# Kernel tuning notes

Hardware: AMD Instinct MI355X
Metric: run time of the kernel (lower is better)

Reference implementation:

```python
import jax, jax.numpy as jnp
import numpy as np

H = 97
IN = 9
N_NODES = 100000
N_EDGES = 800000
N_GRAPHS = 4096
N_LAYERS = 7
N_STEPS = 7
BN_EPS = 1e-5


def setup_inputs() -> dict:
    key = jax.random.key(0)
    ks = iter(jax.random.split(key, 40))
    sc = 0.1  # param init scale
    inp = {}
    inp['x'] = jax.random.normal(next(ks), (N_NODES, IN), jnp.float32)
    inp['edge_index'] = jax.random.randint(next(ks), (2, N_EDGES), 0, N_NODES, jnp.int32)
    inp['batch'] = jnp.sort(jax.random.randint(next(ks), (N_NODES,), 0, N_GRAPHS, jnp.int32))
    inp['num_graphs'] = N_GRAPHS
    inp['lin1_W'] = jax.random.normal(next(ks), (IN, H), jnp.float32) * sc
    inp['lin1_b'] = jax.random.normal(next(ks), (H,), jnp.float32) * sc
    for nm in ['Wk', 'Wq', 'Wv', 'Ws']:
        inp['conv_' + nm] = jax.random.normal(next(ks), (N_LAYERS, H, H), jnp.float32) * sc
    for nm in ['bk', 'bq', 'bv', 'bs']:
        inp['conv_' + nm] = jax.random.normal(next(ks), (N_LAYERS, H), jnp.float32) * sc
    inp['gru_Wih'] = jax.random.normal(next(ks), (N_LAYERS, H, 3 * H), jnp.float32) * sc
    inp['gru_Whh'] = jax.random.normal(next(ks), (N_LAYERS, H, 3 * H), jnp.float32) * sc
    inp['gru_bih'] = jax.random.normal(next(ks), (N_LAYERS, 3 * H), jnp.float32) * sc
    inp['gru_bhh'] = jax.random.normal(next(ks), (N_LAYERS, 3 * H), jnp.float32) * sc
    inp['bn_gamma'] = jnp.ones((N_LAYERS - 1, H), jnp.float32)
    inp['bn_beta'] = jnp.zeros((N_LAYERS - 1, H), jnp.float32)
    inp['bn_mean'] = jnp.zeros((N_LAYERS - 1, H), jnp.float32)
    inp['bn_var'] = jnp.ones((N_LAYERS - 1, H), jnp.float32)
    inp['gat_W'] = jax.random.normal(next(ks), (H, H), jnp.float32) * sc
    inp['gat_asrc'] = jax.random.normal(next(ks), (H,), jnp.float32) * sc
    inp['gat_adst'] = jax.random.normal(next(ks), (H,), jnp.float32) * sc
    inp['gat_b'] = jax.random.normal(next(ks), (H,), jnp.float32) * sc
    inp['molgru_Wih'] = jax.random.normal(next(ks), (H, 3 * H), jnp.float32) * sc
    inp['molgru_Whh'] = jax.random.normal(next(ks), (H, 3 * H), jnp.float32) * sc
    inp['molgru_bih'] = jax.random.normal(next(ks), (3 * H,), jnp.float32) * sc
    inp['molgru_bhh'] = jax.random.normal(next(ks), (3 * H,), jnp.float32) * sc
    inp['lin2_W'] = jax.random.normal(next(ks), (H, 1), jnp.float32) * sc
    inp['lin2_b'] = jax.random.normal(next(ks), (1,), jnp.float32) * sc
    return inp


def _gru(xin, h, Wih, Whh, bih, bhh):
    gi = xin @ Wih + bih  # [N, 3H]
    gh = h @ Whh + bhh
    ir, iz, inn = jnp.split(gi, 3, axis=-1)
    hr, hz, hn = jnp.split(gh, 3, axis=-1)
    r = jax.nn.sigmoid(ir + hr)
    z = jax.nn.sigmoid(iz + hz)
    n = jnp.tanh(inn + r * hn)
    return (1.0 - z) * n + z * h


def _resgated(x, src, dst, Wk, bk, Wq, bq, Wv, bv, Ws, bs, n_nodes):
    # PyG ResGatedGraphConv: out_i = Ws x_i + sum_j sigmoid(Wk x_i + Wq x_j) * (Wv x_j)
    k = x @ Wk + bk
    q = x @ Wq + bq
    v = x @ Wv + bv
    msg = jax.nn.sigmoid(k[dst] + q[src]) * v[src]  # [E, H]
    agg = jax.ops.segment_sum(msg, dst, num_segments=n_nodes)
    return agg + (x @ Ws + bs)


def _forward(x, lin1_W, lin1_b, conv_Wk, conv_bk, conv_Wq, conv_bq, conv_Wv, conv_bv,
             conv_Ws, conv_bs, gru_Wih, gru_Whh, gru_bih, gru_bhh,
             bn_gamma, bn_beta, bn_mean, bn_var,
             gat_W, gat_asrc, gat_adst, gat_b,
             molgru_Wih, molgru_Whh, molgru_bih, molgru_bhh,
             lin2_W, lin2_b, edge_index, batch, num_graphs):
    src, dst = edge_index[0], edge_index[1]
    n_nodes = x.shape[0]
    x = jax.nn.leaky_relu(x @ lin1_W + lin1_b, 0.01)
    # layer 0 (gate_conv + gru)
    h = jax.nn.elu(_resgated(x, src, dst, conv_Wk[0], conv_bk[0], conv_Wq[0], conv_bq[0],
                             conv_Wv[0], conv_bv[0], conv_Ws[0], conv_bs[0], n_nodes))
    x = jax.nn.relu(_gru(h, x, gru_Wih[0], gru_Whh[0], gru_bih[0], gru_bhh[0]))
    # layers 1..6 with eval-mode BatchNorm (dropout inactive in eval)
    for l in range(1, N_LAYERS):
        h = jax.nn.elu(_resgated(x, src, dst, conv_Wk[l], conv_bk[l], conv_Wq[l], conv_bq[l],
                                 conv_Wv[l], conv_bv[l], conv_Ws[l], conv_bs[l], n_nodes))
        b = l - 1
        h = (h - bn_mean[b]) * (bn_gamma[b] / jnp.sqrt(bn_var[b] + BN_EPS)) + bn_beta[b]
        x = jax.nn.relu(_gru(h, x, gru_Wih[l], gru_Whh[l], gru_bih[l], gru_bhh[l]))
    # molecule readout: global_add_pool then bipartite GAT (heads=1) over node->graph edges
    out = jax.nn.relu(jax.ops.segment_sum(x, batch, num_segments=num_graphs))  # [G, H]
    xs = x @ gat_W          # source projections, fixed over timesteps
    a_s = xs @ gat_asrc     # [N]
    for _ in range(N_STEPS):
        a_d = (out @ gat_W) @ gat_adst  # [G]
        alpha = jax.nn.leaky_relu(a_s + a_d[batch], 0.01)  # one score per node-edge
        m = jax.ops.segment_max(alpha, batch, num_segments=num_graphs)
        m = jnp.where(jnp.isfinite(m), m, 0.0)
        e = jnp.exp(alpha - m[batch])
        s = jax.ops.segment_sum(e, batch, num_segments=num_graphs)
        w = e / s[batch]  # segment softmax over each graph's nodes
        hg = jax.ops.segment_sum(w[:, None] * xs, batch, num_segments=num_graphs) + gat_b
        h = jax.nn.elu(hg)
        out = jax.nn.relu(_gru(h, out, molgru_Wih, molgru_Whh, molgru_bih, molgru_bhh))
    return out @ lin2_W + lin2_b  # [G, 1]


def reference(x, edge_index, batch, num_graphs, lin1_W, lin1_b, conv_Wk, conv_bk, conv_Wq,
              conv_bq, conv_Wv, conv_bv, conv_Ws, conv_bs, gru_Wih, gru_Whh, gru_bih, gru_bhh,
              bn_gamma, bn_beta, bn_mean, bn_var, gat_W, gat_asrc, gat_adst, gat_b,
              molgru_Wih, molgru_Whh, molgru_bih, molgru_bhh, lin2_W, lin2_b):
    return _forward(x, lin1_W, lin1_b, conv_Wk, conv_bk, conv_Wq, conv_bq, conv_Wv, conv_bv,
                    conv_Ws, conv_bs, gru_Wih, gru_Whh, gru_bih, gru_bhh,
                    bn_gamma, bn_beta, bn_mean, bn_var,
                    gat_W, gat_asrc, gat_adst, gat_b,
                    molgru_Wih, molgru_Whh, molgru_bih, molgru_bhh,
                    lin2_W, lin2_b, edge_index, batch, num_graphs)
```

## Files before the change

### kernel.cpp

```cpp
#include <hip/hip_runtime.h>

#define NN 100000
#define NNP 100032
#define NE 800000
#define NG 4096
#define HH 97
#define HP 128
#define NB 391

#define WGF_SET_STRIDE 147456
#define WCF_LAYER_STRIDE 98304

typedef unsigned short u16;
typedef unsigned int u32;
typedef __attribute__((ext_vector_type(8))) short short8v;
typedef __attribute__((ext_vector_type(4))) float f32x4;

__device__ __forceinline__ float sigm_(float x){ return 1.f/(1.f+__expf(-x)); }
__device__ __forceinline__ float lrelu01_(float x){ return x>0.f? x : 0.01f*x; }
__device__ __forceinline__ float tanh_(float t){ float e2=__expf(2.f*t); return 1.f-2.f/(e2+1.f); }
__device__ __forceinline__ float b2f(u16 u){ union{u32 i; float f;} t; t.i=(u32)u<<16; return t.f; }
__device__ __forceinline__ u16 f2b(float x){ union{float f; u32 i;} t; t.f=x; u32 r=t.i+0x7FFFu+((t.i>>16)&1u); return (u16)(r>>16); }

__device__ __forceinline__ f32x4 mfma16(short8v a, short8v b, f32x4 c){
  return __builtin_amdgcn_mfma_f32_16x16x32_bf16(a, b, c, 0, 0, 0);
}

__global__ void k_pack_convw(const float* __restrict__ Wk, const float* __restrict__ Wq,
                             const float* __restrict__ Wv, const float* __restrict__ Ws,
                             u16* __restrict__ out){
  int idx = blockIdx.x*256 + threadIdx.x;
  if (idx >= 7*4*8*3*2*512) return;
  int e = idx & 7, lane = (idx>>3) & 63;
  int r = idx >> 9;
  int term = r & 1; r >>= 1;
  int ks = r % 3; r /= 3;
  int t = r & 7; r >>= 3;
  int w = r & 3; int l = r >> 2;
  int k = ks*32 + (lane>>4)*8 + e;
  int n = (w*8 + t)*16 + (lane & 15);
  int m = n>>7, h = n & 127;
  float val = 0.f;
  if (k < HH && h < HH){
    const float* W = (m==0)? Wk : (m==1)? Wq : (m==2)? Wv : Ws;
    val = W[l*9409 + k*97 + h];
  }
  u16 hi = f2b(val);
  out[idx] = (term==0)? hi : f2b(val - b2f(hi));
}

__global__ void k_pack_gruw(const float* __restrict__ gih, const float* __restrict__ ghh,
                            const float* __restrict__ mih, const float* __restrict__ mhh,
                            u16* __restrict__ out){
  int idx = blockIdx.x*256 + threadIdx.x;
  if (idx >= 8*8*3*3*4*512) return;
  int e = idx & 7, lane = (idx>>3) & 63;
  int r = idx >> 9;
  int mat = r & 3; r >>= 2;
  int ks = r % 3; r /= 3;
  int j = r % 3; r /= 3;
  int bt = r & 7; int set = r >> 3;
  int k = ks*32 + (lane>>4)*8 + e;
  int n = (j*8 + bt)*16 + (lane & 15);
  int jg = n>>7, g = n & 127;
  float val = 0.f;
  if (k < HH && g < HH){
    const float* srcp;
    if (mat < 2) srcp = (set < 7)? gih + (size_t)set*28227 : mih;
    else         srcp = (set < 7)? ghh + (size_t)set*28227 : mhh;
    val = srcp[k*291 + jg*97 + g];
  }
  u16 hi = f2b(val);
  out[idx] = ((mat & 1)==0)? hi : f2b(val - b2f(hi));
}

__global__ void k_pack_gatw(const float* __restrict__ gatW, u16* __restrict__ out){
  int idx = blockIdx.x*256 + threadIdx.x;
  if (idx >= 2*4*8*512) return;
  int e = idx & 7, lane = (idx>>3) & 63, t = (idx>>9) & 7;
  int ks = (idx>>12) & 3, term = idx>>14;
  int k = ks*32 + (lane>>4)*8 + e;
  int h = t*16 + (lane & 15);
  float val = (k < HH && h < HH)? gatW[k*97 + h] : 0.f;
  u16 hi = f2b(val);
  out[idx] = (term==0)? hi : f2b(val - b2f(hi));
}

__global__ void k_pack_w96(const float* __restrict__ Wk, const float* __restrict__ Wq,
                           const float* __restrict__ Wv, const float* __restrict__ Ws,
                           const float* __restrict__ gih, const float* __restrict__ ghh,
                           const float* __restrict__ mih, const float* __restrict__ mhh,
                           float* __restrict__ out){
  int idx = blockIdx.x*256 + threadIdx.x;
  if (idx < 7*512){
    int l = idx >> 9, c = idx & 511;
    int m = c >> 7, h = c & 127;
    float v = 0.f;
    if (h < HH){
      const float* W = (m==0)? Wk : (m==1)? Wq : (m==2)? Wv : Ws;
      v = W[l*9409 + 96*97 + h];
    }
    out[idx] = v;
  } else if (idx < 7*512 + 8*384){
    int r = idx - 7*512;
    int set = r / 384, n = r % 384;
    int j = n >> 7, g = n & 127;
    float v = 0.f;
    if (g < HH){
      const float* srcp = (set < 7)? gih + (size_t)set*28227 : mih;
      v = srcp[96*291 + j*97 + g];
    }
    out[idx] = v;
  } else if (idx < 7*512 + 16*384){
    int r = idx - 7*512 - 8*384;
    int set = r / 384, n = r % 384;
    int j = n >> 7, g = n & 127;
    float v = 0.f;
    if (g < HH){
      const float* srcp = (set < 7)? ghh + (size_t)set*28227 : mhh;
      v = srcp[96*291 + j*97 + g];
    }
    out[idx] = v;
  }
}

__global__ void k_pack_convb(const float* __restrict__ bk, const float* __restrict__ bq,
                             const float* __restrict__ bv, const float* __restrict__ bs,
                             float* __restrict__ out){
  int idx = blockIdx.x*256 + threadIdx.x;
  if (idx >= 7*512) return;
  int l = idx >> 9, c = idx & 511;
  int m = c >> 7, h = c & 127;
  float v = 0.f;
  if (h < HH){
    const float* B = (m==0)? bk : (m==1)? bq : (m==2)? bv : bs;
    v = B[l*97 + h];
  }
  out[idx] = v;
}

__global__ void k_pack_grub(const float* __restrict__ gbi, const float* __restrict__ gbh,
                            const float* __restrict__ mbi, const float* __restrict__ mbh,
                            float* __restrict__ obi, float* __restrict__ obh){
  int idx = blockIdx.x*256 + threadIdx.x;
  if (idx >= 8*384) return;
  int set = idx / 384, n = idx % 384;
  int j = n>>7, g = n & 127;
  float vi = 0.f, vh = 0.f;
  if (g < HH){
    const float* si = (set < 7)? gbi + set*291 : mbi;
    const float* sh = (set < 7)? gbh + set*291 : mbh;
    vi = si[j*97 + g];
    vh = sh[j*97 + g];
  }
  obi[idx] = vi; obh[idx] = vh;
}

__global__ void k_pack_misc(const float* __restrict__ gatW, const float* __restrict__ asrc,
                            const float* __restrict__ adst, const float* __restrict__ gatb,
                            const float* __restrict__ l2W, float* __restrict__ out){
  int idx = blockIdx.x*256 + threadIdx.x;
  if (idx < 16384){
    int k = idx >> 7, h = idx & 127;
    out[idx] = (k < HH && h < HH)? gatW[k*97 + h] : 0.f;
  } else if (idx < 16512){
    int h = idx - 16384; out[idx] = (h < HH)? asrc[h] : 0.f;
  } else if (idx < 16640){
    int h = idx - 16512; out[idx] = (h < HH)? adst[h] : 0.f;
  } else if (idx < 16768){
    int h = idx - 16640; out[idx] = (h < HH)? gatb[h] : 0.f;
  } else if (idx < 16896){
    int h = idx - 16768; out[idx] = (h < HH)? l2W[h] : 0.f;
  } else if (idx < 17408){
    out[idx] = 0.f;
  }
}

__global__ void k_seg(const int* __restrict__ batch, int* __restrict__ seg){
  int g = blockIdx.x*blockDim.x + threadIdx.x;
  if (g > NG) return;
  int lo = 0, hi = NN;
  while (lo < hi){ int mid = (lo+hi) >> 1; if (batch[mid] < g) lo = mid+1; else hi = mid; }
  seg[g] = lo;
}

__global__ void k_hist(const int* __restrict__ dst, int* __restrict__ cnt){
  int e = blockIdx.x*256 + threadIdx.x;
  if (e < NE) atomicAdd(&cnt[dst[e]], 1);
}

__global__ void k_scan_blk(const int* __restrict__ cnt, int* __restrict__ offs,
                           int* __restrict__ bsum){
  __shared__ int s[256];
  int b = blockIdx.x, t = threadIdx.x, i = b*256 + t;
  int v = (i < NN)? cnt[i] : 0;
  s[t] = v; __syncthreads();
  #pragma unroll
  for (int off = 1; off < 256; off <<= 1){
    int tmp = (t >= off)? s[t-off] : 0;
    __syncthreads();
    s[t] += tmp;
    __syncthreads();
  }
  if (i < NN) offs[i] = s[t] - v;
  if (t == 255) bsum[b] = s[255];
}

__global__ void k_scan_top(int* __restrict__ bsum){
  __shared__ int s[512];
  int t = threadIdx.x;
  int v = (t < NB)? bsum[t] : 0;
  s[t] = v; __syncthreads();
  #pragma unroll
  for (int off = 1; off < 512; off <<= 1){
    int tmp = (t >= off)? s[t-off] : 0;
    __syncthreads();
    s[t] += tmp;
    __syncthreads();
  }
  if (t < NB) bsum[t] = s[t] - v;
}

__global__ void k_scan_add(int* __restrict__ offs, const int* __restrict__ bsum,
                           int* __restrict__ cur){
  int b = blockIdx.x, t = threadIdx.x, i = b*256 + t;
  if (i < NN){ int o = offs[i] + bsum[b]; offs[i] = o; cur[i] = o; }
  if (i == 0) offs[NN] = NE;
}

__global__ void k_scatter(const int* __restrict__ src, const int* __restrict__ dst,
                          int* __restrict__ cur, int* __restrict__ eidx){
  int e = blockIdx.x*256 + threadIdx.x;
  if (e >= NE) return;
  int pos = atomicAdd(&cur[dst[e]], 1);
  eidx[pos] = src[e];
}

__global__ __launch_bounds__(256) void k_lin1(const float* __restrict__ x,
    const float* __restrict__ W, const float* __restrict__ b, u16* __restrict__ X0){
  int idx = blockIdx.x*256 + threadIdx.x;
  int n = idx >> 7, c = idx & 127;
  float v = 0.f;
  if (n < NN && c < HH){
    v = b[c];
    #pragma unroll
    for (int k = 0; k < 9; ++k) v += x[n*9 + k]*W[k*HH + c];
    v = lrelu01_(v);
  }
  X0[(size_t)n*HP + c] = f2b(v);
}

__global__ __launch_bounds__(256) void k_conv_mfma(const u16* __restrict__ X,
    const u16* __restrict__ WCF_l, const float* __restrict__ biasp,
    const float* __restrict__ W96C, u16* __restrict__ KQV,
    u16* __restrict__ Sh, u16* __restrict__ Sl){
  int tid = threadIdx.x;
  int w = __builtin_amdgcn_readfirstlane(tid >> 6);
  int lane = tid & 63;
  int lm = lane & 15, ls = lane >> 4;
  int m0 = blockIdx.x*64;
  f32x4 acc[4][8] = {};
  const u16* pw = WCF_l + (size_t)w*24576 + lane*8;
  for (int ks = 0; ks < 3; ++ks){
    short8v aX[4];
    #pragma unroll
    for (int rb = 0; rb < 4; ++rb)
      aX[rb] = *(const short8v*)(X + (size_t)(m0 + rb*16 + lm)*HP + ks*32 + ls*8);
    short8v wf[8][2];
    #pragma unroll
    for (int t = 0; t < 8; ++t){
      const u16* q = pw + ((t*3 + ks) << 10);
      wf[t][0] = *(const short8v*)(q);
      wf[t][1] = *(const short8v*)(q + 512);
    }
    #pragma unroll
    for (int t = 0; t < 8; ++t)
      #pragma unroll
      for (int rb = 0; rb < 4; ++rb){
        acc[rb][t] = mfma16(aX[rb], wf[t][0], acc[rb][t]);
        acc[rb][t] = mfma16(aX[rb], wf[t][1], acc[rb][t]);
      }
  }
  float x96[4][4];
  #pragma unroll
  for (int rb = 0; rb < 4; ++rb)
    #pragma unroll
    for (int r = 0; r < 4; ++r)
      x96[rb][r] = b2f(X[(size_t)(m0 + rb*16 + ls*4 + r)*HP + 96]);
  #pragma unroll
  for (int t = 0; t < 8; ++t){
    int c = t*16 + lm;
    int col = w*128 + c;
    float bv = biasp[col];
    float w96 = W96C[col];
    #pragma unroll
    for (int rb = 0; rb < 4; ++rb)
      #pragma unroll
      for (int r = 0; r < 4; ++r){
        int row = m0 + rb*16 + ls*4 + r;
        float v = acc[rb][t][r] + bv + x96[rb][r]*w96;
        if (w < 3) KQV[(size_t)row*384 + w*128 + c] = f2b(v);
        else {
          u16 hb = f2b(v);
          Sh[(size_t)row*HP + c] = hb;
          Sl[(size_t)row*HP + c] = f2b(v - b2f(hb));
        }
      }
  }
}

__global__ __launch_bounds__(256) void k_gru_mfma(const u16* __restrict__ Sh_,
    const u16* __restrict__ Sl_, const u16* __restrict__ Xin,
    const u16* __restrict__ WGF_set,
    const float* __restrict__ bihp, const float* __restrict__ bhhp,
    const float* __restrict__ W96I, const float* __restrict__ W96H,
    u16* __restrict__ Xout){
  int tid = threadIdx.x;
  int w = __builtin_amdgcn_readfirstlane(tid >> 6);
  int lane = tid & 63;
  int lm = lane & 15, ls = lane >> 4;
  int m0 = blockIdx.x*64;
  f32x4 agi[4][2][3] = {};
  f32x4 agh[4][2][3] = {};
  for (int ks = 0; ks < 3; ++ks){
    short8v aX[4], aSh[4], aSl[4];
    #pragma unroll
    for (int rb = 0; rb < 4; ++rb){
      size_t off = (size_t)(m0 + rb*16 + lm)*HP + ks*32 + ls*8;
      aX[rb]  = *(const short8v*)(Xin + off);
      aSh[rb] = *(const short8v*)(Sh_ + off);
      aSl[rb] = *(const short8v*)(Sl_ + off);
    }
    #pragma unroll
    for (int b = 0; b < 2; ++b){
      const u16* pb = WGF_set + (size_t)(2*w + b)*18432 + lane*8;
      short8v fIh[3], fIl[3], fHh[3], fHl[3];
      #pragma unroll
      for (int j = 0; j < 3; ++j){
        const u16* q = pb + ((j*3 + ks) << 11);
        fIh[j] = *(const short8v*)(q);
        fIl[j] = *(const short8v*)(q + 512);
        fHh[j] = *(const short8v*)(q + 1024);
        fHl[j] = *(const short8v*)(q + 1536);
      }
      #pragma unroll
      for (int j = 0; j < 3; ++j)
        #pragma unroll
        for (int rb = 0; rb < 4; ++rb){
          agi[rb][b][j] = mfma16(aSh[rb], fIh[j], agi[rb][b][j]);
          agi[rb][b][j] = mfma16(aSh[rb], fIl[j], agi[rb][b][j]);
          agi[rb][b][j] = mfma16(aSl[rb], fIh[j], agi[rb][b][j]);
          agh[rb][b][j] = mfma16(aX[rb], fHh[j], agh[rb][b][j]);
          agh[rb][b][j] = mfma16(aX[rb], fHl[j], agh[rb][b][j]);
        }
    }
  }
  float s96[4][4], x96[4][4];
  #pragma unroll
  for (int rb = 0; rb < 4; ++rb)
    #pragma unroll
    for (int r = 0; r < 4; ++r){
      size_t o96 = (size_t)(m0 + rb*16 + ls*4 + r)*HP + 96;
      s96[rb][r] = b2f(Sh_[o96]) + b2f(Sl_[o96]);
      x96[rb][r] = b2f(Xin[o96]);
    }
  #pragma unroll
  for (int b = 0; b < 2; ++b){
    int g = (2*w + b)*16 + lm;
    float bi0 = bihp[g], bi1 = bihp[128+g], bi2 = bihp[256+g];
    float bh0 = bhhp[g], bh1 = bhhp[128+g], bh2 = bhhp[256+g];
    float wi0 = W96I[g], wi1 = W96I[128+g], wi2 = W96I[256+g];
    float wh0 = W96H[g], wh1 = W96H[128+g], wh2 = W96H[256+g];
    #pragma unroll
    for (int rb = 0; rb < 4; ++rb)
      #pragma unroll
      for (int r = 0; r < 4; ++r){
        int row = m0 + rb*16 + ls*4 + r;
        float ir = agi[rb][b][0][r] + bi0 + s96[rb][r]*wi0;
        float iz = agi[rb][b][1][r] + bi1 + s96[rb][r]*wi1;
        float in_ = agi[rb][b][2][r] + bi2 + s96[rb][r]*wi2;
        float hr = agh[rb][b][0][r] + bh0 + x96[rb][r]*wh0;
        float hz = agh[rb][b][1][r] + bh1 + x96[rb][r]*wh1;
        float hn = agh[rb][b][2][r] + bh2 + x96[rb][r]*wh2;
        float rr = sigm_(ir + hr);
        float zz = sigm_(iz + hz);
        float nn2 = tanh_(in_ + rr*hn);
        float xo = b2f(Xin[(size_t)row*HP + g]);
        float v = (1.f - zz)*nn2 + zz*xo;
        Xout[(size_t)row*HP + g] = f2b(fmaxf(v, 0.f));
      }
  }
}

__global__ __launch_bounds__(256) void k_xs_mfma(const u16* __restrict__ X,
    const u16* __restrict__ GATF, u16* __restrict__ XS){
  int tid = threadIdx.x;
  int w = tid >> 6, lane = tid & 63;
  int lm = lane & 15, ls = lane >> 4;
  int m0 = blockIdx.x*32;
  f32x4 acc[2][2] = {};
  for (int ks = 0; ks < 4; ++ks){
    short8v aX[2];
    #pragma unroll
    for (int rb = 0; rb < 2; ++rb){
      int row = m0 + rb*16 + lm;
      aX[rb] = *(const short8v*)(X + (size_t)row*HP + ks*32 + ls*8);
    }
    #pragma unroll
    for (int b = 0; b < 2; ++b){
      int t = 2*w + b;
      short8v bh = *(const short8v*)(GATF + (((size_t)(0*4 + ks)*8 + t)*64 + lane)*8);
      short8v bl = *(const short8v*)(GATF + (((size_t)(1*4 + ks)*8 + t)*64 + lane)*8);
      #pragma unroll
      for (int rb = 0; rb < 2; ++rb){
        acc[rb][b] = mfma16(aX[rb], bh, acc[rb][b]);
        acc[rb][b] = mfma16(aX[rb], bl, acc[rb][b]);
      }
    }
  }
  #pragma unroll
  for (int b = 0; b < 2; ++b){
    int c = (2*w + b)*16 + lm;
    #pragma unroll
    for (int rb = 0; rb < 2; ++rb)
      #pragma unroll
      for (int r = 0; r < 4; ++r){
        int row = m0 + rb*16 + ls*4 + r;
        XS[(size_t)row*HP + c] = f2b(acc[rb][b][r]);
      }
  }
}

__global__ __launch_bounds__(256) void k_agg(const u16* __restrict__ kqv,
    const int* __restrict__ offs, const int* __restrict__ eidx,
    u16* __restrict__ Sh, u16* __restrict__ Sl,
    const float* __restrict__ gamma, const float* __restrict__ beta,
    const float* __restrict__ mean, const float* __restrict__ var, int layer){
  int n = blockIdx.x*4 + (threadIdx.x >> 6);
  if (n >= NN) return;
  int lane = threadIdx.x & 63;
  int c2 = lane*2;
  int lo = offs[n], hi = offs[n+1];
  ushort2 kk = *(const ushort2*)(kqv + (size_t)n*384 + c2);
  float k0 = b2f(kk.x), k1 = b2f(kk.y);
  float a0 = 0.f, a1 = 0.f;
  int i = lo;
  for (; i + 4 <= hi; i += 4){
    int s0 = eidx[i], s1 = eidx[i+1], s2 = eidx[i+2], s3 = eidx[i+3];
    const u16* q0 = kqv + (size_t)s0*384 + 128 + c2;
    const u16* q1 = kqv + (size_t)s1*384 + 128 + c2;
    const u16* q2 = kqv + (size_t)s2*384 + 128 + c2;
    const u16* q3 = kqv + (size_t)s3*384 + 128 + c2;
    ushort2 qa = *(const ushort2*)q0, va = *(const ushort2*)(q0 + 128);
    ushort2 qb = *(const ushort2*)q1, vb = *(const ushort2*)(q1 + 128);
    ushort2 qc = *(const ushort2*)q2, vc = *(const ushort2*)(q2 + 128);
    ushort2 qd = *(const ushort2*)q3, vd = *(const ushort2*)(q3 + 128);
    a0 += b2f(va.x)*sigm_(k0 + b2f(qa.x)); a1 += b2f(va.y)*sigm_(k1 + b2f(qa.y));
    a0 += b2f(vb.x)*sigm_(k0 + b2f(qb.x)); a1 += b2f(vb.y)*sigm_(k1 + b2f(qb.y));
    a0 += b2f(vc.x)*sigm_(k0 + b2f(qc.x)); a1 += b2f(vc.y)*sigm_(k1 + b2f(qc.y));
    a0 += b2f(vd.x)*sigm_(k0 + b2f(qd.x)); a1 += b2f(vd.y)*sigm_(k1 + b2f(qd.y));
  }
  for (; i < hi; ++i){
    int s = eidx[i];
    const u16* qb0 = kqv + (size_t)s*384 + 128 + c2;
    ushort2 qq = *(const ushort2*)qb0;
    ushort2 vv = *(const ushort2*)(qb0 + 128);
    a0 += b2f(vv.x)*sigm_(k0 + b2f(qq.x));
    a1 += b2f(vv.y)*sigm_(k1 + b2f(qq.y));
  }
  u16* shp = Sh + (size_t)n*HP + c2;
  u16* slp = Sl + (size_t)n*HP + c2;
  ushort2 sh2 = *(const ushort2*)shp;
  ushort2 sl2 = *(const ushort2*)slp;
  float v0 = b2f(sh2.x) + b2f(sl2.x) + a0;
  float v1 = b2f(sh2.y) + b2f(sl2.y) + a1;
  v0 = v0 > 0.f ? v0 : (__expf(v0) - 1.f);
  v1 = v1 > 0.f ? v1 : (__expf(v1) - 1.f);
  if (layer > 0){
    int b0 = (layer-1)*97 + c2;
    if (c2 < HH){ float sc = gamma[b0]*rsqrtf(var[b0] + 1e-5f); v0 = (v0 - mean[b0])*sc + beta[b0]; }
    if (c2+1 < HH){ float sc = gamma[b0+1]*rsqrtf(var[b0+1] + 1e-5f); v1 = (v1 - mean[b0+1])*sc + beta[b0+1]; }
  }
  if (c2 >= HH)   v0 = 0.f;
  if (c2+1 >= HH) v1 = 0.f;
  u16 h0 = f2b(v0), h1 = f2b(v1);
  *(ushort2*)shp = make_ushort2(h0, h1);
  *(ushort2*)slp = make_ushort2(f2b(v0 - b2f(h0)), f2b(v1 - b2f(h1)));
}

__global__ __launch_bounds__(128) void k_pool(const int* __restrict__ seg,
    const u16* __restrict__ x, u16* __restrict__ out){
  int g = blockIdx.x, tid = threadIdx.x;
  int lo = seg[g], hi = seg[g+1];
  float acc = 0.f;
  for (int n = lo; n < hi; ++n) acc += b2f(x[(size_t)n*HP + tid]);
  out[(size_t)g*HP + tid] = f2b(fmaxf(acc, 0.f));
}

__global__ __launch_bounds__(256) void k_as(const u16* __restrict__ xs,
    const float* __restrict__ asrcp, float* __restrict__ a_s){
  int t = blockIdx.x*256 + threadIdx.x;
  int n = t >> 6, lane = t & 63;
  float v = b2f(xs[(size_t)n*HP + lane])*asrcp[lane]
          + b2f(xs[(size_t)n*HP + 64 + lane])*asrcp[64 + lane];
  #pragma unroll
  for (int o = 32; o > 0; o >>= 1) v += __shfl_down(v, o);
  if (lane == 0) a_s[n] = v;
}

__global__ __launch_bounds__(128) void k_ad(const u16* __restrict__ out,
    const float* __restrict__ gatwp, const float* __restrict__ adstp, float* __restrict__ ad){
  int g = blockIdx.x, tid = threadIdx.x;
  __shared__ float so[HP];
  __shared__ float red[2];
  so[tid] = b2f(out[(size_t)g*HP + tid]);
  __syncthreads();
  float p = 0.f;
  #pragma unroll 4
  for (int k = 0; k < HP; ++k) p += so[k]*gatwp[k*HP + tid];
  float v = p * adstp[tid];
  #pragma unroll
  for (int o = 32; o > 0; o >>= 1) v += __shfl_down(v, o);
  if ((tid & 63) == 0) red[tid >> 6] = v;
  __syncthreads();
  if (tid == 0) ad[g] = red[0] + red[1];
}

#define ACAP 2048
__global__ __launch_bounds__(128) void k_attn(const int* __restrict__ seg,
    const float* __restrict__ a_s, const float* __restrict__ a_d,
    const u16* __restrict__ xs, const float* __restrict__ gbp,
    u16* __restrict__ hgh, u16* __restrict__ hgl){
  int g = blockIdx.x, tid = threadIdx.x;
  int lo = seg[g], hi = seg[g+1], cnt = hi - lo;
  float ad = a_d[g];
  __shared__ float sa[ACAP];
  __shared__ float red[2];
  float mloc = -3.4e38f;
  for (int i = tid; i < cnt; i += 128){
    float al = lrelu01_(a_s[lo+i] + ad);
    if (i < ACAP) sa[i] = al;
    mloc = fmaxf(mloc, al);
  }
  #pragma unroll
  for (int o = 32; o > 0; o >>= 1) mloc = fmaxf(mloc, __shfl_down(mloc, o));
  if ((tid & 63) == 0) red[tid >> 6] = mloc;
  __syncthreads();
  float mm = fmaxf(red[0], red[1]);
  __syncthreads();
  float sloc = 0.f;
  for (int i = tid; i < cnt; i += 128){
    float al = (i < ACAP)? sa[i] : lrelu01_(a_s[lo+i] + ad);
    float e = __expf(al - mm);
    if (i < ACAP) sa[i] = e;
    sloc += e;
  }
  #pragma unroll
  for (int o = 32; o > 0; o >>= 1) sloc += __shfl_down(sloc, o);
  if ((tid & 63) == 0) red[tid >> 6] = sloc;
  __syncthreads();
  float ss = red[0] + red[1];
  float inv = (cnt > 0 && ss != 0.f)? 1.f/ss : 0.f;
  __syncthreads();
  float accv = 0.f;
  for (int i = 0; i < cnt; ++i){
    float e = (i < ACAP)? sa[i] : __expf(lrelu01_(a_s[lo+i] + ad) - mm);
    accv += (e*inv) * b2f(xs[(size_t)(lo+i)*HP + tid]);
  }
  float hgv = accv + gbp[tid];
  hgv = hgv > 0.f ? hgv : (__expf(hgv) - 1.f);
  u16 hb = f2b(hgv);
  hgh[(size_t)g*HP + tid] = hb;
  hgl[(size_t)g*HP + tid] = f2b(hgv - b2f(hb));
}

__global__ __launch_bounds__(64) void k_final(const u16* __restrict__ out,
    const float* __restrict__ w2p, const float* __restrict__ l2b, float* __restrict__ y){
  int g = blockIdx.x, lane = threadIdx.x;
  float v = b2f(out[(size_t)g*HP + lane])*w2p[lane]
          + b2f(out[(size_t)g*HP + 64 + lane])*w2p[64 + lane];
  #pragma unroll
  for (int o = 32; o > 0; o >>= 1) v += __shfl_down(v, o);
  if (lane == 0) y[g] = v + l2b[0];
}

extern "C" void kernel_launch(void* const* d_in, const int* in_sizes, int n_in,
                              void* d_out, int out_size, void* d_ws, size_t ws_size,
                              hipStream_t stream){
  const float* x_in  = (const float*)d_in[0];
  const int*   ei    = (const int*)d_in[1];
  const int*   batch = (const int*)d_in[2];
  const float* lin1W = (const float*)d_in[4];
  const float* lin1b = (const float*)d_in[5];
  const float* cWk = (const float*)d_in[6];
  const float* cWq = (const float*)d_in[7];
  const float* cWv = (const float*)d_in[8];
  const float* cWs = (const float*)d_in[9];
  const float* cbk = (const float*)d_in[10];
  const float* cbq = (const float*)d_in[11];
  const float* cbv = (const float*)d_in[12];
  const float* cbs = (const float*)d_in[13];
  const float* gWih = (const float*)d_in[14];
  const float* gWhh = (const float*)d_in[15];
  const float* gbih = (const float*)d_in[16];
  const float* gbhh = (const float*)d_in[17];
  const float* bng = (const float*)d_in[18];
  const float* bnb = (const float*)d_in[19];
  const float* bnm = (const float*)d_in[20];
  const float* bnv = (const float*)d_in[21];
  const float* gatW  = (const float*)d_in[22];
  const float* gasrc = (const float*)d_in[23];
  const float* gadst = (const float*)d_in[24];
  const float* gatb  = (const float*)d_in[25];
  const float* mWih = (const float*)d_in[26];
  const float* mWhh = (const float*)d_in[27];
  const float* mbih = (const float*)d_in[28];
  const float* mbhh = (const float*)d_in[29];
  const float* l2W = (const float*)d_in[30];
  const float* l2b = (const float*)d_in[31];
  const int* src = ei;
  const int* dst = ei + NE;

  char* base = (char*)d_ws;
  size_t off = 0;
  auto alloc = [&](size_t nbytes)->char*{
    char* p = base + off; off = (off + nbytes + 255) & ~(size_t)255; return p; };

  u16*  WCF  = (u16*)alloc((size_t)7*WCF_LAYER_STRIDE*2);
  u16*  WGF  = (u16*)alloc((size_t)8*WGF_SET_STRIDE*2);
  u16*  GATF = (u16*)alloc((size_t)2*4*8*512*2);
  float* W96  = (float*)alloc((size_t)(7*512 + 16*384)*4);
  float* BCONVP = (float*)alloc(7*512*4);
  float* BIHP   = (float*)alloc(8*384*4);
  float* BHHP   = (float*)alloc(8*384*4);
  float* GATWP  = (float*)alloc(17408*4);
  float* ASRCP = GATWP + 16384;
  float* ADSTP = GATWP + 16512;
  float* GBP   = GATWP + 16640;
  float* W2P   = GATWP + 16768;
  u16*  X0  = (u16*)alloc((size_t)NNP*HP*2);
  u16*  X1  = (u16*)alloc((size_t)NNP*HP*2);
  u16*  KQV = (u16*)alloc((size_t)NNP*384*2);
  u16*  Sh  = (u16*)alloc((size_t)NNP*HP*2);
  u16*  Sl  = (u16*)alloc((size_t)NNP*HP*2);
  float* AS_ = (float*)alloc((size_t)NN*4);
  float* AD_ = (float*)alloc((size_t)NG*4);
  u16*  OUTA = (u16*)alloc((size_t)NG*HP*2);
  u16*  OUTB = (u16*)alloc((size_t)NG*HP*2);
  u16*  HGH  = (u16*)alloc((size_t)NG*HP*2);
  u16*  HGL  = (u16*)alloc((size_t)NG*HP*2);
  int*  SEG  = (int*)alloc((size_t)(NG+1)*4);
  int*  CNT  = (int*)alloc((size_t)NN*4);
  int*  OFFS = (int*)alloc((size_t)(NN+1)*4);
  int*  CUR  = (int*)alloc((size_t)NN*4);
  int*  EIDX = (int*)alloc((size_t)NE*4);
  int*  BSUM = (int*)alloc((size_t)NB*4);

  float* W96C = W96;
  float* W96I = W96 + 7*512;
  float* W96H = W96 + 7*512 + 8*384;

  if (ws_size < off){
    hipMemsetAsync(d_out, 0, (size_t)out_size*sizeof(float), stream);
    return;
  }

  k_pack_convw<<<(7*WCF_LAYER_STRIDE)/256,256,0,stream>>>(cWk,cWq,cWv,cWs,WCF);
  k_pack_gruw<<<(8*WGF_SET_STRIDE)/256,256,0,stream>>>(gWih,gWhh,mWih,mWhh,WGF);
  k_pack_gatw<<<(2*4*8*512+255)/256,256,0,stream>>>(gatW,GATF);
  k_pack_w96<<<(7*512+16*384+255)/256,256,0,stream>>>(cWk,cWq,cWv,cWs,gWih,gWhh,mWih,mWhh,W96);
  k_pack_convb<<<(7*512+255)/256,256,0,stream>>>(cbk,cbq,cbv,cbs,BCONVP);
  k_pack_grub<<<(8*384+255)/256,256,0,stream>>>(gbih,gbhh,mbih,mbhh,BIHP,BHHP);
  k_pack_misc<<<68,256,0,stream>>>(gatW,gasrc,gadst,gatb,l2W,GATWP);
  k_lin1<<<(NNP*HP)/256,256,0,stream>>>(x_in,lin1W,lin1b,X0);
  k_seg<<<(NG+1+255)/256,256,0,stream>>>(batch,SEG);

  hipMemsetAsync(CNT, 0, (size_t)NN*4, stream);
  k_hist<<<(NE+255)/256,256,0,stream>>>(dst, CNT);
  k_scan_blk<<<NB,256,0,stream>>>(CNT, OFFS, BSUM);
  k_scan_top<<<1,512,0,stream>>>(BSUM);
  k_scan_add<<<NB,256,0,stream>>>(OFFS, BSUM, CUR);
  k_scatter<<<(NE+255)/256,256,0,stream>>>(src, dst, CUR, EIDX);

  for (int l = 0; l < 7; ++l){
    u16* Xin  = (l & 1)? X1 : X0;
    u16* Xout = (l & 1)? X0 : X1;
    k_conv_mfma<<<NNP/64,256,0,stream>>>(Xin, WCF + (size_t)l*WCF_LAYER_STRIDE,
                                         BCONVP + l*512, W96C + l*512, KQV, Sh, Sl);
    k_agg<<<(NN+3)/4,256,0,stream>>>(KQV, OFFS, EIDX, Sh, Sl, bng, bnb, bnm, bnv, l);
    k_gru_mfma<<<NNP/64,256,0,stream>>>(Sh, Sl, Xin, WGF + (size_t)l*WGF_SET_STRIDE,
                                        BIHP + l*384, BHHP + l*384,
                                        W96I + l*384, W96H + l*384, Xout);
  }
  u16* XF = X1;

  k_pool<<<NG,128,0,stream>>>(SEG, XF, OUTA);
  u16* XS = KQV;
  k_xs_mfma<<<NNP/32,256,0,stream>>>(XF, GATF, XS);
  k_as<<<(NN*64)/256,256,0,stream>>>(XS, ASRCP, AS_);

  u16* cur = OUTA; u16* nxt = OUTB;
  for (int s = 0; s < 7; ++s){
    k_ad<<<NG,128,0,stream>>>(cur, GATWP, ADSTP, AD_);
    k_attn<<<NG,128,0,stream>>>(SEG, AS_, AD_, XS, GBP, HGH, HGL);
    k_gru_mfma<<<NG/64,256,0,stream>>>(HGH, HGL, cur, WGF + (size_t)7*WGF_SET_STRIDE,
                                       BIHP + 7*384, BHHP + 7*384,
                                       W96I + 7*384, W96H + 7*384, nxt);
    u16* t = cur; cur = nxt; nxt = t;
  }
  k_final<<<NG,64,0,stream>>>(cur, W2P, l2b, (float*)d_out);
}
```

Before: 2.613 ms.

## Swap MFMA operands for row-contiguous outputs and halve GRU tile rows

The MFMA operand order is swapped in the conv, GRU and xs kernels. Each lane's accumulator then holds four consecutive output columns for a single node, so epilogue stores become 8-byte ushort4 writes instead of scattered 2-byte writes, and bias/weight loads become float4. The GRU kernel also processes 32 rows per block instead of 64, which doubles the grid and cuts accumulator register pressure at the cost of reloading weights more often.

```diff
diff --git a/kernel.cpp b/kernel.cpp
--- a/kernel.cpp
+++ b/kernel.cpp
@@ -21,6 +21,11 @@
 __device__ __forceinline__ float tanh_(float t){ float e2=__expf(2.f*t); return 1.f-2.f/(e2+1.f); }
 __device__ __forceinline__ float b2f(u16 u){ union{u32 i; float f;} t; t.i=(u32)u<<16; return t.f; }
 __device__ __forceinline__ u16 f2b(float x){ union{float f; u32 i;} t; t.f=x; u32 r=t.i+0x7FFFu+((t.i>>16)&1u); return (u16)(r>>16); }
+
+__device__ __forceinline__ void store_bf16x4(u16* p, float v0, float v1, float v2, float v3){
+  ushort4 s; s.x = f2b(v0); s.y = f2b(v1); s.z = f2b(v2); s.w = f2b(v3);
+  *(ushort4*)p = s;
+}
 
 __device__ __forceinline__ f32x4 mfma16(short8v a, short8v b, f32x4 c){
   return __builtin_amdgcn_mfma_f32_16x16x32_bf16(a, b, c, 0, 0, 0);
@@ -277,35 +282,37 @@
     for (int t = 0; t < 8; ++t)
       #pragma unroll
       for (int rb = 0; rb < 4; ++rb){
-        acc[rb][t] = mfma16(aX[rb], wf[t][0], acc[rb][t]);
-        acc[rb][t] = mfma16(aX[rb], wf[t][1], acc[rb][t]);
+        acc[rb][t] = mfma16(wf[t][0], aX[rb], acc[rb][t]);
+        acc[rb][t] = mfma16(wf[t][1], aX[rb], acc[rb][t]);
       }
   }
-  float x96[4][4];
+  float x96[4];
   #pragma unroll
   for (int rb = 0; rb < 4; ++rb)
-    #pragma unroll
-    for (int r = 0; r < 4; ++r)
-      x96[rb][r] = b2f(X[(size_t)(m0 + rb*16 + ls*4 + r)*HP + 96]);
+    x96[rb] = b2f(X[(size_t)(m0 + rb*16 + lm)*HP + 96]);
   #pragma unroll
   for (int t = 0; t < 8; ++t){
-    int c = t*16 + lm;
-    int col = w*128 + c;
-    float bv = biasp[col];
-    float w96 = W96C[col];
-    #pragma unroll
-    for (int rb = 0; rb < 4; ++rb)
-      #pragma unroll
-      for (int r = 0; r < 4; ++r){
-        int row = m0 + rb*16 + ls*4 + r;
-        float v = acc[rb][t][r] + bv + x96[rb][r]*w96;
-        if (w < 3) KQV[(size_t)row*384 + w*128 + c] = f2b(v);
-        else {
-          u16 hb = f2b(v);
-          Sh[(size_t)row*HP + c] = hb;
-          Sl[(size_t)row*HP + c] = f2b(v - b2f(hb));
-        }
+    int c0 = w*128 + t*16 + ls*4;
+    float4 bv = *(const float4*)(biasp + c0);
+    float4 w96 = *(const float4*)(W96C + c0);
+    #pragma unroll
+    for (int rb = 0; rb < 4; ++rb){
+      int node = m0 + rb*16 + lm;
+      float v0 = acc[rb][t][0] + bv.x + x96[rb]*w96.x;
+      float v1 = acc[rb][t][1] + bv.y + x96[rb]*w96.y;
+      float v2 = acc[rb][t][2] + bv.z + x96[rb]*w96.z;
+      float v3 = acc[rb][t][3] + bv.w + x96[rb]*w96.w;
+      if (w < 3){
+        store_bf16x4(KQV + (size_t)node*384 + w*128 + t*16 + ls*4, v0, v1, v2, v3);
+      } else {
+        int co = t*16 + ls*4;
+        u16 h0 = f2b(v0), h1 = f2b(v1), h2 = f2b(v2), h3 = f2b(v3);
+        ushort4 hv; hv.x=h0; hv.y=h1; hv.z=h2; hv.w=h3;
+        *(ushort4*)(Sh + (size_t)node*HP + co) = hv;
+        store_bf16x4(Sl + (size_t)node*HP + co,
+                     v0 - b2f(h0), v1 - b2f(h1), v2 - b2f(h2), v3 - b2f(h3));
       }
+    }
   }
 }
 
@@ -319,13 +326,13 @@
   int w = __builtin_amdgcn_readfirstlane(tid >> 6);
   int lane = tid & 63;
   int lm = lane & 15, ls = lane >> 4;
-  int m0 = blockIdx.x*64;
-  f32x4 agi[4][2][3] = {};
-  f32x4 agh[4][2][3] = {};
+  int m0 = blockIdx.x*32;
+  f32x4 agi[2][2][3] = {};
+  f32x4 agh[2][2][3] = {};
   for (int ks = 0; ks < 3; ++ks){
-    short8v aX[4], aSh[4], aSl[4];
-    #pragma unroll
-    for (int rb = 0; rb < 4; ++rb){
+    short8v aX[2], aSh[2], aSl[2];
+    #pragma unroll
+    for (int rb = 0; rb < 2; ++rb){
       size_t off = (size_t)(m0 + rb*16 + lm)*HP + ks*32 + ls*8;
       aX[rb]  = *(const short8v*)(Xin + off);
       aSh[rb] = *(const short8v*)(Sh_ + off);
@@ -346,49 +353,63 @@
       #pragma unroll
       for (int j = 0; j < 3; ++j)
         #pragma unroll
-        for (int rb = 0; rb < 4; ++rb){
-          agi[rb][b][j] = mfma16(aSh[rb], fIh[j], agi[rb][b][j]);
-          agi[rb][b][j] = mfma16(aSh[rb], fIl[j], agi[rb][b][j]);
-          agi[rb][b][j] = mfma16(aSl[rb], fIh[j], agi[rb][b][j]);
-          agh[rb][b][j] = mfma16(aX[rb], fHh[j], agh[rb][b][j]);
-          agh[rb][b][j] = mfma16(aX[rb], fHl[j], agh[rb][b][j]);
+        for (int rb = 0; rb < 2; ++rb){
+          agi[rb][b][j] = mfma16(fIh[j], aSh[rb], agi[rb][b][j]);
+          agi[rb][b][j] = mfma16(fIl[j], aSh[rb], agi[rb][b][j]);
+          agi[rb][b][j] = mfma16(fIh[j], aSl[rb], agi[rb][b][j]);
+          agh[rb][b][j] = mfma16(fHh[j], aX[rb], agh[rb][b][j]);
+          agh[rb][b][j] = mfma16(fHl[j], aX[rb], agh[rb][b][j]);
         }
     }
   }
-  float s96[4][4], x96[4][4];
-  #pragma unroll
-  for (int rb = 0; rb < 4; ++rb)
-    #pragma unroll
-    for (int r = 0; r < 4; ++r){
-      size_t o96 = (size_t)(m0 + rb*16 + ls*4 + r)*HP + 96;
-      s96[rb][r] = b2f(Sh_[o96]) + b2f(Sl_[o96]);
-      x96[rb][r] = b2f(Xin[o96]);
-    }
+  float s96[2], x96[2];
+  #pragma unroll
+  for (int rb = 0; rb < 2; ++rb){
+    size_t o96 = (size_t)(m0 + rb*16 + lm)*HP + 96;
+    s96[rb] = b2f(Sh_[o96]) + b2f(Sl_[o96]);
+    x96[rb] = b2f(Xin[o96]);
+  }
   #pragma unroll
   for (int b = 0; b < 2; ++b){
-    int g = (2*w + b)*16 + lm;
-    float bi0 = bihp[g], bi1 = bihp[128+g], bi2 = bihp[256+g];
-    float bh0 = bhhp[g], bh1 = bhhp[128+g], bh2 = bhhp[256+g];
-    float wi0 = W96I[g], wi1 = W96I[128+g], wi2 = W96I[256+g];
-    float wh0 = W96H[g], wh1 = W96H[128+g], wh2 = W96H[256+g];
-    #pragma unroll
-    for (int rb = 0; rb < 4; ++rb)
+    int g0 = (2*w + b)*16 + ls*4;
+    float4 bi0 = *(const float4*)(bihp + g0);
+    float4 bi1 = *(const float4*)(bihp + 128 + g0);
+    float4 bi2 = *(const float4*)(bihp + 256 + g0);
+    float4 bh0 = *(const float4*)(bhhp + g0);
+    float4 bh1 = *(const float4*)(bhhp + 128 + g0);
+    float4 bh2 = *(const float4*)(bhhp + 256 + g0);
+    float4 wi0 = *(const float4*)(W96I + g0);
+    float4 wi1 = *(const float4*)(W96I + 128 + g0);
+    float4 wi2 = *(const float4*)(W96I + 256 + g0);
+    float4 wh0 = *(const float4*)(W96H + g0);
+    float4 wh1 = *(const float4*)(W96H + 128 + g0);
+    float4 wh2 = *(const float4*)(W96H + 256 + g0);
+    #pragma unroll
+    for (int rb = 0; rb < 2; ++rb){
+      int node = m0 + rb*16 + lm;
+      ushort4 xo4 = *(const ushort4*)(Xin + (size_t)node*HP + g0);
+      float xo[4] = { b2f(xo4.x), b2f(xo4.y), b2f(xo4.z), b2f(xo4.w) };
+      float vout[4];
       #pragma unroll
       for (int r = 0; r < 4; ++r){
-        int row = m0 + rb*16 + ls*4 + r;
-        float ir = agi[rb][b][0][r] + bi0 + s96[rb][r]*wi0;
-        float iz = agi[rb][b][1][r] + bi1 + s96[rb][r]*wi1;
-        float in_ = agi[rb][b][2][r] + bi2 + s96[rb][r]*wi2;
-        float hr = agh[rb][b][0][r] + bh0 + x96[rb][r]*wh0;
-        float hz = agh[rb][b][1][r] + bh1 + x96[rb][r]*wh1;
-        float hn = agh[rb][b][2][r] + bh2 + x96[rb][r]*wh2;
+        float biv0 = ((const float*)&bi0)[r], biv1 = ((const float*)&bi1)[r], biv2 = ((const float*)&bi2)[r];
+        float bhv0 = ((const float*)&bh0)[r], bhv1 = ((const float*)&bh1)[r], bhv2 = ((const float*)&bh2)[r];
+        float wiv0 = ((const float*)&wi0)[r], wiv1 = ((const float*)&wi1)[r], wiv2 = ((const float*)&wi2)[r];
+        float whv0 = ((const float*)&wh0)[r], whv1 = ((const float*)&wh1)[r], whv2 = ((const float*)&wh2)[r];
+        float ir = agi[rb][b][0][r] + biv0 + s96[rb]*wiv0;
+        float iz = agi[rb][b][1][r] + biv1 + s96[rb]*wiv1;
+        float in_ = agi[rb][b][2][r] + biv2 + s96[rb]*wiv2;
+        float hr = agh[rb][b][0][r] + bhv0 + x96[rb]*whv0;
+        float hz = agh[rb][b][1][r] + bhv1 + x96[rb]*whv1;
+        float hn = agh[rb][b][2][r] + bhv2 + x96[rb]*whv2;
         float rr = sigm_(ir + hr);
         float zz = sigm_(iz + hz);
         float nn2 = tanh_(in_ + rr*hn);
-        float xo = b2f(Xin[(size_t)row*HP + g]);
-        float v = (1.f - zz)*nn2 + zz*xo;
-        Xout[(size_t)row*HP + g] = f2b(fmaxf(v, 0.f));
+        float v = (1.f - zz)*nn2 + zz*xo[r];
+        vout[r] = fmaxf(v, 0.f);
       }
+      store_bf16x4(Xout + (size_t)node*HP + g0, vout[0], vout[1], vout[2], vout[3]);
+    }
   }
 }
 
@@ -413,21 +434,20 @@
       short8v bl = *(const short8v*)(GATF + (((size_t)(1*4 + ks)*8 + t)*64 + lane)*8);
       #pragma unroll
       for (int rb = 0; rb < 2; ++rb){
-        acc[rb][b] = mfma16(aX[rb], bh, acc[rb][b]);
-        acc[rb][b] = mfma16(aX[rb], bl, acc[rb][b]);
+        acc[rb][b] = mfma16(bh, aX[rb], acc[rb][b]);
+        acc[rb][b] = mfma16(bl, aX[rb], acc[rb][b]);
       }
     }
   }
   #pragma unroll
   for (int b = 0; b < 2; ++b){
-    int c = (2*w + b)*16 + lm;
-    #pragma unroll
-    for (int rb = 0; rb < 2; ++rb)
-      #pragma unroll
-      for (int r = 0; r < 4; ++r){
-        int row = m0 + rb*16 + ls*4 + r;
-        XS[(size_t)row*HP + c] = f2b(acc[rb][b][r]);
-      }
+    int c0 = (2*w + b)*16 + ls*4;
+    #pragma unroll
+    for (int rb = 0; rb < 2; ++rb){
+      int node = m0 + rb*16 + lm;
+      store_bf16x4(XS + (size_t)node*HP + c0,
+                   acc[rb][b][0], acc[rb][b][1], acc[rb][b][2], acc[rb][b][3]);
+    }
   }
 }
 
@@ -688,7 +708,7 @@
     k_conv_mfma<<<NNP/64,256,0,stream>>>(Xin, WCF + (size_t)l*WCF_LAYER_STRIDE,
                                          BCONVP + l*512, W96C + l*512, KQV, Sh, Sl);
     k_agg<<<(NN+3)/4,256,0,stream>>>(KQV, OFFS, EIDX, Sh, Sl, bng, bnb, bnm, bnv, l);
-    k_gru_mfma<<<NNP/64,256,0,stream>>>(Sh, Sl, Xin, WGF + (size_t)l*WGF_SET_STRIDE,
+    k_gru_mfma<<<NNP/32,256,0,stream>>>(Sh, Sl, Xin, WGF + (size_t)l*WGF_SET_STRIDE,
                                         BIHP + l*384, BHHP + l*384,
                                         W96I + l*384, W96H + l*384, Xout);
   }
@@ -703,7 +723,7 @@
   for (int s = 0; s < 7; ++s){
     k_ad<<<NG,128,0,stream>>>(cur, GATWP, ADSTP, AD_);
     k_attn<<<NG,128,0,stream>>>(SEG, AS_, AD_, XS, GBP, HGH, HGL);
-    k_gru_mfma<<<NG/64,256,0,stream>>>(HGH, HGL, cur, WGF + (size_t)7*WGF_SET_STRIDE,
+    k_gru_mfma<<<NG/32,256,0,stream>>>(HGH, HGL, cur, WGF + (size_t)7*WGF_SET_STRIDE,
                                        BIHP + 7*384, BHHP + 7*384,
                                        W96I + 7*384, W96H + 7*384, nxt);
     u16* t = cur; cur = nxt; nxt = t;
```

Measured after the change: 2.722 ms. +4.2%, slower.
